# Kernel tuning notes

Hardware: AMD Instinct MI355X
Metric: run time of the kernel (lower is better)

The kernel has to match this reference:

```python
import jax, jax.numpy as jnp
import numpy as np

REG = 1.0
NITERS = 50

def setup_inputs() -> dict:
    key = jax.random.key(0)
    B, N = 256, 512
    cost = jax.random.uniform(key, (B, N, N), dtype=jnp.float32)
    return {"cost": cost}

def reference(cost) -> jnp.ndarray:
    B, N, _ = cost.shape
    K = jnp.exp(-REG * cost)                      # [B, N, N] Gibbs kernel
    u0 = jnp.ones((B, N), dtype=cost.dtype) / N
    v0 = jnp.ones((B, N), dtype=cost.dtype) / N

    def body(carry, _):
        u, v = carry
        v = 1.0 / jnp.einsum('ki,kij->kj', u, K)  # column scaling
        u = 1.0 / jnp.einsum('kij,kj->ki', K, v)  # row scaling
        return (u, v), None

    (u, v), _ = jax.lax.scan(body, (u0, v0), None, length=NITERS)
    P = u[:, :, None] * K * v[:, None, :]         # [B, N, N]
    return jnp.log(P)
```

## Files before the change

kernel.cpp:

```cpp
#include <hip/hip_runtime.h>


#define SK_B   256
#define SK_N   512
#define SK_NIT 50
#define SK_LR  112

__device__ __forceinline__ unsigned short f2bf_rne(float f) {
    union { float f; unsigned int u; } x; x.f = f;
    unsigned int r = (x.u + 0x7FFFu + ((x.u >> 16) & 1u)) >> 16;
    return (unsigned short)r;
}
__device__ __forceinline__ float bf_lo(unsigned int u) {
    union { unsigned int u; float f; } x; x.u = u << 16; return x.f;
}
__device__ __forceinline__ float bf_hi(unsigned int u) {
    union { unsigned int u; float f; } x; x.u = u & 0xffff0000u; return x.f;
}

__global__ void k_makeK(const float4* __restrict__ cost, ushort4* __restrict__ K, int n4) {
    int stride = gridDim.x * blockDim.x;
    for (int i = blockIdx.x * blockDim.x + threadIdx.x; i < n4; i += stride) {
        float4 c = cost[i];
        ushort4 o;
        o.x = f2bf_rne(__expf(-c.x));
        o.y = f2bf_rne(__expf(-c.y));
        o.z = f2bf_rne(__expf(-c.z));
        o.w = f2bf_rne(__expf(-c.w));
        K[i] = o;
    }
}

#define SK_UNPACK(p) \
    const float k0 = bf_lo((p).x), k1 = bf_hi((p).x), k2 = bf_lo((p).y), k3 = bf_hi((p).y), \
                k4 = bf_lo((p).z), k5 = bf_hi((p).z), k6 = bf_lo((p).w), k7 = bf_hi((p).w)

#define SK_DOT_RED(sv) \
    float sv; { \
        float s0_ = k0 * vv0; s0_ = fmaf(k2, vv2, s0_); s0_ = fmaf(k4, vv4, s0_); s0_ = fmaf(k6, vv6, s0_); \
        float s1_ = k1 * vv1; s1_ = fmaf(k3, vv3, s1_); s1_ = fmaf(k5, vv5, s1_); s1_ = fmaf(k7, vv7, s1_); \
        sv = s0_ + s1_; \
        sv += __shfl_xor(sv, 32, 64); sv += __shfl_xor(sv, 16, 64); sv += __shfl_xor(sv, 8, 64); \
        sv += __shfl_xor(sv, 4, 64);  sv += __shfl_xor(sv, 2, 64);  sv += __shfl_xor(sv, 1, 64); \
    }

#define SK_LOADVV() \
    const float vv0 = v_s[lane*8+0], vv1 = v_s[lane*8+1], \
                vv2 = v_s[lane*8+2], vv3 = v_s[lane*8+3], \
                vv4 = v_s[lane*8+4], vv5 = v_s[lane*8+5], \
                vv6 = v_s[lane*8+6], vv7 = v_s[lane*8+7]

#define SK_ACCUM(ui) \
    a0 = fmaf((ui), k0, a0); a1 = fmaf((ui), k1, a1); a2 = fmaf((ui), k2, a2); a3 = fmaf((ui), k3, a3); \
    a4 = fmaf((ui), k4, a4); a5 = fmaf((ui), k5, a5); a6 = fmaf((ui), k6, a6); a7 = fmaf((ui), k7, a7)

__launch_bounds__(1024)
__global__ void k_sinkhorn(const unsigned short* __restrict__ Kg,
                           float* __restrict__ lu, float* __restrict__ lv) {
    const int b = blockIdx.x;
    const uint4* __restrict__ Kb = (const uint4*)(Kg + (size_t)b * SK_N * SK_N);
    __shared__ uint4 Kl[SK_LR * 64];
    __shared__ float part[16][SK_N];
    __shared__ float v_s[SK_N];
    const int tid  = threadIdx.x;
    const int lane = tid & 63;
    const int w    = tid >> 6;

    {
        float a0=0.f,a1=0.f,a2=0.f,a3=0.f,a4=0.f,a5=0.f,a6=0.f,a7=0.f;
        for (int i = w; i < SK_N; i += 16) {
            uint4 p = Kb[i * 64 + lane];
            if (i < SK_LR) Kl[i * 64 + lane] = p;
            SK_UNPACK(p);
            a0 += k0; a1 += k1; a2 += k2; a3 += k3;
            a4 += k4; a5 += k5; a6 += k6; a7 += k7;
        }
        float* pr = &part[w][lane * 8];
        pr[0]=a0; pr[1]=a1; pr[2]=a2; pr[3]=a3; pr[4]=a4; pr[5]=a5; pr[6]=a6; pr[7]=a7;
        __syncthreads();
        if (tid < SK_N) {
            float s = 0.f;
            #pragma unroll
            for (int g = 0; g < 16; ++g) s += part[g][tid];
            v_s[tid] = __builtin_amdgcn_rcpf(s * (1.0f / SK_N));
        }
        __syncthreads();
    }

    for (int t = 1; t < SK_NIT; ++t) {
        SK_LOADVV();
        float a0=0.f,a1=0.f,a2=0.f,a3=0.f,a4=0.f,a5=0.f,a6=0.f,a7=0.f;
        for (int i = w; i < SK_LR; i += 16) {
            uint4 p = Kl[i * 64 + lane];
            SK_UNPACK(p);
            SK_DOT_RED(s);
            const float ui = __builtin_amdgcn_rcpf(s);
            SK_ACCUM(ui);
        }
        uint4 pg = Kb[(SK_LR + w) * 64 + lane];
        for (int i = SK_LR + w; i < SK_N; i += 16) {
            const uint4 p = pg;
            if (i + 16 < SK_N) pg = Kb[(i + 16) * 64 + lane];
            SK_UNPACK(p);
            SK_DOT_RED(s);
            const float ui = __builtin_amdgcn_rcpf(s);
            SK_ACCUM(ui);
        }
        float* pr = &part[w][lane * 8];
        pr[0]=a0; pr[1]=a1; pr[2]=a2; pr[3]=a3; pr[4]=a4; pr[5]=a5; pr[6]=a6; pr[7]=a7;
        __syncthreads();
        if (tid < SK_N) {
            float s = 0.f;
            #pragma unroll
            for (int g = 0; g < 16; ++g) s += part[g][tid];
            v_s[tid] = __builtin_amdgcn_rcpf(s);
        }
        __syncthreads();
    }

    {
        SK_LOADVV();
        for (int i = w; i < SK_LR; i += 16) {
            uint4 p = Kl[i * 64 + lane];
            SK_UNPACK(p);
            SK_DOT_RED(s);
            if (lane == 0) lu[b * SK_N + i] = -__logf(s);
        }
        for (int i = SK_LR + w; i < SK_N; i += 16) {
            uint4 p = Kb[i * 64 + lane];
            SK_UNPACK(p);
            SK_DOT_RED(s);
            if (lane == 0) lu[b * SK_N + i] = -__logf(s);
        }
        if (tid < SK_N) lv[b * SK_N + tid] = __logf(v_s[tid]);
    }
}

__global__ void k_out(const float4* __restrict__ cost, const float* __restrict__ lu,
                      const float4* __restrict__ lv4, float4* __restrict__ out, int n4) {
    int idx = blockIdx.x * blockDim.x + threadIdx.x;
    if (idx >= n4) return;
    int bb  = idx >> 16;
    int row = (idx >> 7) & (SK_N - 1);
    int j4  = idx & 127;
    float  l_u = lu[bb * SK_N + row];
    float4 lvv = lv4[bb * 128 + j4];
    float4 c   = cost[idx];
    float4 o;
    o.x = l_u - c.x + lvv.x;
    o.y = l_u - c.y + lvv.y;
    o.z = l_u - c.z + lvv.z;
    o.w = l_u - c.w + lvv.w;
    out[idx] = o;
}

extern "C" void kernel_launch(void* const* d_in, const int* in_sizes, int n_in,
                              void* d_out, int out_size, void* d_ws, size_t ws_size,
                              hipStream_t stream) {
    const float* cost = (const float*)d_in[0];
    float* out = (float*)d_out;

    unsigned short* K = (unsigned short*)d_out;
    float* lu = (float*)d_ws;
    float* lv = lu + SK_B * SK_N;

    const int n4 = SK_B * SK_N * SK_N / 4;

    k_makeK<<<8192, 256, 0, stream>>>((const float4*)cost, (ushort4*)K, n4);
    k_sinkhorn<<<SK_B, 1024, 0, stream>>>(K, lu, lv);
    k_out<<<n4 / 256, 256, 0, stream>>>((const float4*)cost, lu,
                                        (const float4*)lv, (float4*)out, n4);
}
```

Measured before the change: 1.232 ms.

## Fuse Gibbs kernel construction into Sinkhorn and cache rows in registers

After: 4.359 ms. 3.54x slower.

```diff
diff --git a/kernel.cpp b/kernel.cpp
--- a/kernel.cpp
+++ b/kernel.cpp
@@ -1,47 +1,37 @@
 #include <hip/hip_runtime.h>
 
 
-#define SK_B   256
-#define SK_N   512
-#define SK_NIT 50
-#define SK_LR  112
-
-__device__ __forceinline__ unsigned short f2bf_rne(float f) {
-    union { float f; unsigned int u; } x; x.f = f;
-    unsigned int r = (x.u + 0x7FFFu + ((x.u >> 16) & 1u)) >> 16;
-    return (unsigned short)r;
-}
+#define SK_B    256
+#define SK_N    512
+#define SK_NIT  50
+#define SK_RREG 13
+#define SK_GST  20
+
 __device__ __forceinline__ float bf_lo(unsigned int u) {
     union { unsigned int u; float f; } x; x.u = u << 16; return x.f;
 }
 __device__ __forceinline__ float bf_hi(unsigned int u) {
     union { unsigned int u; float f; } x; x.u = u & 0xffff0000u; return x.f;
 }
-
-__global__ void k_makeK(const float4* __restrict__ cost, ushort4* __restrict__ K, int n4) {
-    int stride = gridDim.x * blockDim.x;
-    for (int i = blockIdx.x * blockDim.x + threadIdx.x; i < n4; i += stride) {
-        float4 c = cost[i];
-        ushort4 o;
-        o.x = f2bf_rne(__expf(-c.x));
-        o.y = f2bf_rne(__expf(-c.y));
-        o.z = f2bf_rne(__expf(-c.z));
-        o.w = f2bf_rne(__expf(-c.w));
-        K[i] = o;
-    }
-}
-
-#define SK_UNPACK(p) \
-    const float k0 = bf_lo((p).x), k1 = bf_hi((p).x), k2 = bf_lo((p).y), k3 = bf_hi((p).y), \
-                k4 = bf_lo((p).z), k5 = bf_hi((p).z), k6 = bf_lo((p).w), k7 = bf_hi((p).w)
-
-#define SK_DOT_RED(sv) \
-    float sv; { \
-        float s0_ = k0 * vv0; s0_ = fmaf(k2, vv2, s0_); s0_ = fmaf(k4, vv4, s0_); s0_ = fmaf(k6, vv6, s0_); \
-        float s1_ = k1 * vv1; s1_ = fmaf(k3, vv3, s1_); s1_ = fmaf(k5, vv5, s1_); s1_ = fmaf(k7, vv7, s1_); \
-        sv = s0_ + s1_; \
-        sv += __shfl_xor(sv, 32, 64); sv += __shfl_xor(sv, 16, 64); sv += __shfl_xor(sv, 8, 64); \
-        sv += __shfl_xor(sv, 4, 64);  sv += __shfl_xor(sv, 2, 64);  sv += __shfl_xor(sv, 1, 64); \
+__device__ __forceinline__ unsigned int pk2bf(float a, float b) {
+    union { float f; unsigned int u; } x, y; x.f = a; y.f = b;
+    unsigned int ra = (x.u + 0x7FFFu + ((x.u >> 16) & 1u)) >> 16;
+    unsigned int rb = (y.u + 0x7FFFu + ((y.u >> 16) & 1u)) & 0xFFFF0000u;
+    return ra | rb;
+}
+__device__ __forceinline__ float rdlane(float v, int l) {
+    return __uint_as_float(__builtin_amdgcn_readlane(__float_as_uint(v), l));
+}
+
+#define SK_UNP(p, n0,n1,n2,n3,n4,n5,n6,n7) \
+    const float n0 = bf_lo((p).x), n1 = bf_hi((p).x), n2 = bf_lo((p).y), n3 = bf_hi((p).y), \
+                n4 = bf_lo((p).z), n5 = bf_hi((p).z), n6 = bf_lo((p).w), n7 = bf_hi((p).w)
+
+#define SK_DOT(s, n0,n1,n2,n3,n4,n5,n6,n7) \
+    float s; { \
+        float e_ = n0 * vv0; e_ = fmaf(n2, vv2, e_); e_ = fmaf(n4, vv4, e_); e_ = fmaf(n6, vv6, e_); \
+        float o_ = n1 * vv1; o_ = fmaf(n3, vv3, o_); o_ = fmaf(n5, vv5, o_); o_ = fmaf(n7, vv7, o_); \
+        s = e_ + o_; \
     }
 
 #define SK_LOADVV() \
@@ -50,38 +40,68 @@
                 vv4 = v_s[lane*8+4], vv5 = v_s[lane*8+5], \
                 vv6 = v_s[lane*8+6], vv7 = v_s[lane*8+7]
 
-#define SK_ACCUM(ui) \
-    a0 = fmaf((ui), k0, a0); a1 = fmaf((ui), k1, a1); a2 = fmaf((ui), k2, a2); a3 = fmaf((ui), k3, a3); \
-    a4 = fmaf((ui), k4, a4); a5 = fmaf((ui), k5, a5); a6 = fmaf((ui), k6, a6); a7 = fmaf((ui), k7, a7)
+#define SK_FETCH(p, r, pfreg) \
+    uint4 p; \
+    if ((r) < SK_RREG)     p = kreg[(r)]; \
+    else if ((r) < SK_GST) p = Kl[(((r) - SK_RREG) * 16 + w) * 64 + lane]; \
+    else                   p = pfreg;
+
+#define SK_RED2(xx, sA, sB) \
+    float xx; { \
+        float x_ = (lane & 1) ? sB : sA; \
+        float y_ = (lane & 1) ? sA : sB; \
+        x_ += __shfl_xor(y_, 1, 64); \
+        x_ += __shfl_xor(x_, 2, 64); \
+        x_ += __shfl_xor(x_, 4, 64); \
+        x_ += __shfl_xor(x_, 8, 64); \
+        x_ += __shfl_xor(x_, 16, 64); \
+        x_ += __shfl_xor(x_, 32, 64); \
+        xx = x_; \
+    }
 
 __launch_bounds__(1024)
-__global__ void k_sinkhorn(const unsigned short* __restrict__ Kg,
+__global__ void k_sinkhorn(const float* __restrict__ cost,
+                           unsigned short* __restrict__ Kg,
                            float* __restrict__ lu, float* __restrict__ lv) {
     const int b = blockIdx.x;
-    const uint4* __restrict__ Kb = (const uint4*)(Kg + (size_t)b * SK_N * SK_N);
-    __shared__ uint4 Kl[SK_LR * 64];
+    const float4* __restrict__ costb = (const float4*)(cost + (size_t)b * SK_N * SK_N);
+    uint4* __restrict__ Kb = (uint4*)(Kg + (size_t)b * SK_N * SK_N);
+    __shared__ uint4 Kl[(SK_GST - SK_RREG) * 16 * 64];
     __shared__ float part[16][SK_N];
     __shared__ float v_s[SK_N];
     const int tid  = threadIdx.x;
     const int lane = tid & 63;
     const int w    = tid >> 6;
 
+    uint4 kreg[SK_RREG];
+
     {
         float a0=0.f,a1=0.f,a2=0.f,a3=0.f,a4=0.f,a5=0.f,a6=0.f,a7=0.f;
-        for (int i = w; i < SK_N; i += 16) {
-            uint4 p = Kb[i * 64 + lane];
-            if (i < SK_LR) Kl[i * 64 + lane] = p;
-            SK_UNPACK(p);
-            a0 += k0; a1 += k1; a2 += k2; a3 += k3;
-            a4 += k4; a5 += k5; a6 += k6; a7 += k7;
+        #pragma unroll
+        for (int r = 0; r < 32; ++r) {
+            const int i = w + 16 * r;
+            const float4 c0 = costb[i * 128 + 2 * lane];
+            const float4 c1 = costb[i * 128 + 2 * lane + 1];
+            uint4 kp;
+            kp.x = pk2bf(__expf(-c0.x), __expf(-c0.y));
+            kp.y = pk2bf(__expf(-c0.z), __expf(-c0.w));
+            kp.z = pk2bf(__expf(-c1.x), __expf(-c1.y));
+            kp.w = pk2bf(__expf(-c1.z), __expf(-c1.w));
+            if (r < SK_RREG)     kreg[r] = kp;
+            else if (r < SK_GST) Kl[((r - SK_RREG) * 16 + w) * 64 + lane] = kp;
+            else                 Kb[i * 64 + lane] = kp;
+            SK_UNP(kp, k0,k1,k2,k3,k4,k5,k6,k7);
+            a0+=k0; a1+=k1; a2+=k2; a3+=k3; a4+=k4; a5+=k5; a6+=k6; a7+=k7;
         }
         float* pr = &part[w][lane * 8];
         pr[0]=a0; pr[1]=a1; pr[2]=a2; pr[3]=a3; pr[4]=a4; pr[5]=a5; pr[6]=a6; pr[7]=a7;
         __syncthreads();
         if (tid < SK_N) {
-            float s = 0.f;
-            #pragma unroll
-            for (int g = 0; g < 16; ++g) s += part[g][tid];
+            float t0 = part[0][tid] + part[1][tid],   t1 = part[2][tid] + part[3][tid];
+            float t2 = part[4][tid] + part[5][tid],   t3 = part[6][tid] + part[7][tid];
+            float t4 = part[8][tid] + part[9][tid],   t5 = part[10][tid] + part[11][tid];
+            float t6 = part[12][tid] + part[13][tid], t7 = part[14][tid] + part[15][tid];
+            float s = ((t0+t1)+(t2+t3)) + ((t4+t5)+(t6+t7));
             v_s[tid] = __builtin_amdgcn_rcpf(s * (1.0f / SK_N));
         }
         __syncthreads();
@@ -90,29 +110,43 @@
     for (int t = 1; t < SK_NIT; ++t) {
         SK_LOADVV();
         float a0=0.f,a1=0.f,a2=0.f,a3=0.f,a4=0.f,a5=0.f,a6=0.f,a7=0.f;
-        for (int i = w; i < SK_LR; i += 16) {
-            uint4 p = Kl[i * 64 + lane];
-            SK_UNPACK(p);
-            SK_DOT_RED(s);
-            const float ui = __builtin_amdgcn_rcpf(s);
-            SK_ACCUM(ui);
-        }
-        uint4 pg = Kb[(SK_LR + w) * 64 + lane];
-        for (int i = SK_LR + w; i < SK_N; i += 16) {
-            const uint4 p = pg;
-            if (i + 16 < SK_N) pg = Kb[(i + 16) * 64 + lane];
-            SK_UNPACK(p);
-            SK_DOT_RED(s);
-            const float ui = __builtin_amdgcn_rcpf(s);
-            SK_ACCUM(ui);
+        uint4 pfa = Kb[(w + 16 * SK_GST) * 64 + lane];
+        uint4 pfb = Kb[(w + 16 * (SK_GST + 1)) * 64 + lane];
+        #pragma unroll
+        for (int g = 0; g < 16; ++g) {
+            const int r0 = 2 * g, r1 = r0 + 1;
+            SK_FETCH(p0, r0, pfa);
+            SK_FETCH(p1, r1, pfb);
+            if (r0 >= SK_GST && r0 + 2 < 32) {
+                pfa = Kb[(w + 16 * (r0 + 2)) * 64 + lane];
+                pfb = Kb[(w + 16 * (r1 + 2)) * 64 + lane];
+            }
+            SK_UNP(p0, A0,A1,A2,A3,A4,A5,A6,A7);
+            SK_UNP(p1, B0,B1,B2,B3,B4,B5,B6,B7);
+            SK_DOT(sA, A0,A1,A2,A3,A4,A5,A6,A7);
+            SK_DOT(sB, B0,B1,B2,B3,B4,B5,B6,B7);
+            SK_RED2(xx, sA, sB);
+            const float uu = __builtin_amdgcn_rcpf(xx);
+            const float uA = rdlane(uu, 0);
+            const float uB = rdlane(uu, 1);
+            a0 = fmaf(uA, A0, fmaf(uB, B0, a0));
+            a1 = fmaf(uA, A1, fmaf(uB, B1, a1));
+            a2 = fmaf(uA, A2, fmaf(uB, B2, a2));
+            a3 = fmaf(uA, A3, fmaf(uB, B3, a3));
+            a4 = fmaf(uA, A4, fmaf(uB, B4, a4));
+            a5 = fmaf(uA, A5, fmaf(uB, B5, a5));
+            a6 = fmaf(uA, A6, fmaf(uB, B6, a6));
+            a7 = fmaf(uA, A7, fmaf(uB, B7, a7));
         }
         float* pr = &part[w][lane * 8];
         pr[0]=a0; pr[1]=a1; pr[2]=a2; pr[3]=a3; pr[4]=a4; pr[5]=a5; pr[6]=a6; pr[7]=a7;
         __syncthreads();
         if (tid < SK_N) {
-            float s = 0.f;
-            #pragma unroll
-            for (int g = 0; g < 16; ++g) s += part[g][tid];
+            float t0 = part[0][tid] + part[1][tid],   t1 = part[2][tid] + part[3][tid];
+            float t2 = part[4][tid] + part[5][tid],   t3 = part[6][tid] + part[7][tid];
+            float t4 = part[8][tid] + part[9][tid],   t5 = part[10][tid] + part[11][tid];
+            float t6 = part[12][tid] + part[13][tid], t7 = part[14][tid] + part[15][tid];
+            float s = ((t0+t1)+(t2+t3)) + ((t4+t5)+(t6+t7));
             v_s[tid] = __builtin_amdgcn_rcpf(s);
         }
         __syncthreads();
@@ -120,17 +154,24 @@
 
     {
         SK_LOADVV();
-        for (int i = w; i < SK_LR; i += 16) {
-            uint4 p = Kl[i * 64 + lane];
-            SK_UNPACK(p);
-            SK_DOT_RED(s);
-            if (lane == 0) lu[b * SK_N + i] = -__logf(s);
-        }
-        for (int i = SK_LR + w; i < SK_N; i += 16) {
-            uint4 p = Kb[i * 64 + lane];
-            SK_UNPACK(p);
-            SK_DOT_RED(s);
-            if (lane == 0) lu[b * SK_N + i] = -__logf(s);
+        uint4 pfa = Kb[(w + 16 * SK_GST) * 64 + lane];
+        uint4 pfb = Kb[(w + 16 * (SK_GST + 1)) * 64 + lane];
+        #pragma unroll
+        for (int g = 0; g < 16; ++g) {
+            const int r0 = 2 * g, r1 = r0 + 1;
+            SK_FETCH(p0, r0, pfa);
+            SK_FETCH(p1, r1, pfb);
+            if (r0 >= SK_GST && r0 + 2 < 32) {
+                pfa = Kb[(w + 16 * (r0 + 2)) * 64 + lane];
+                pfb = Kb[(w + 16 * (r1 + 2)) * 64 + lane];
+            }
+            SK_UNP(p0, A0,A1,A2,A3,A4,A5,A6,A7);
+            SK_UNP(p1, B0,B1,B2,B3,B4,B5,B6,B7);
+            SK_DOT(sA, A0,A1,A2,A3,A4,A5,A6,A7);
+            SK_DOT(sB, B0,B1,B2,B3,B4,B5,B6,B7);
+            SK_RED2(xx, sA, sB);
+            if (lane < 2)
+                lu[b * SK_N + w + 16 * (r0 + lane)] = -__logf(xx);
         }
         if (tid < SK_N) lv[b * SK_N + tid] = __logf(v_s[tid]);
     }
@@ -166,8 +207,7 @@
 
     const int n4 = SK_B * SK_N * SK_N / 4;
 
-    k_makeK<<<8192, 256, 0, stream>>>((const float4*)cost, (ushort4*)K, n4);
-    k_sinkhorn<<<SK_B, 1024, 0, stream>>>(K, lu, lv);
+    k_sinkhorn<<<SK_B, 1024, 0, stream>>>(cost, K, lu, lv);
     k_out<<<n4 / 256, 256, 0, stream>>>((const float4*)cost, lu,
                                         (const float4*)lv, (float4*)out, n4);
 }
```
